# Kernel optimization log

Hardware: AMD Instinct MI355X
Metric: run time of the kernel (lower is better)

Reference implementation:

```python
import jax, jax.numpy as jnp
import numpy as np

jax.config.update("jax_enable_x64", True)  # original torch code runs in float64; minors underflow fp32

D = 96   # Nsites
N = 48   # Nparticles


def setup_inputs() -> dict:
    key = jax.random.key(0)
    # Orthonormal single-particle orbitals (columns), as the module assumes (P^T P = I)
    A = jax.random.normal(key, (D, D), dtype=jnp.float64)
    Q, _ = jnp.linalg.qr(A)
    P = Q[:, :N]  # [D, N]
    # A valid ordered particle configuration: strictly increasing, occ_positions[k] <= D-N+k
    occ_positions = jnp.arange(N, dtype=jnp.int32) * (D // N)  # stride-2 filling
    return {"P": P, "occ_positions": occ_positions}


def _cond_probs(P, occ_positions):
    """Conditional probabilities probs[k, x] of placing the k-th (ordered) particle at
    site x given particles 0..k-1 at occ_positions[0..k-1].

    Math identical to SlaterDetSampler_ordered.get_cond_prob (naive_update=True):
      G = I - P P^T
      probs[k,x] = -det(M_x[0:x+1,0:x+1]) / det(M[0:xmin,0:xmin])
    where M = G - diag(occupancy of particles < k) and M_x additionally sets n_x = 1.
    Since Ksites is always the contiguous range 0..x, all determinants are LEADING
    principal minors; and because only the (x,x) diagonal entry changes by -1 (last index
    of the block), det(M_x block) = d_{x+1} - d_x with d_j the leading j-minor of M.
    """
    Dd, Nn = P.shape
    dt = P.dtype
    eye = jnp.eye(Dd, dtype=dt)
    G = eye - P @ P.T                                             # [D, D]

    onehots = jax.nn.one_hot(occ_positions, Dd, dtype=dt)         # [N, D]
    n_before = jnp.cumsum(onehots, axis=0) - onehots              # occupancy of particles < k
    A = G[None] - n_before[:, :, None] * eye                      # [N, D, D]: G - diag(n_<k)

    # All leading principal minors via batched det of masked matrices:
    # M_j = A on the [0:j,0:j] block, identity elsewhere  =>  det(M_j) = leading j-minor
    ii = jnp.arange(Dd)
    jj = jnp.arange(1, Dd + 1)
    blk = (ii[None, :, None] < jj[:, None, None]) & (ii[None, None, :] < jj[:, None, None])  # [D,D,D]
    Ms = jnp.where(blk[None], A[:, None], eye)                    # [N, D, D, D]
    d = jnp.linalg.det(Ms.reshape(Nn * Dd, Dd, Dd)).reshape(Nn, Dd)
    d_full = jnp.concatenate([jnp.ones((Nn, 1), dt), d], axis=1)  # d_full[k, j] = j-th leading minor

    k = jnp.arange(Nn)
    xmin = jnp.where(k == 0, 0, occ_positions[jnp.maximum(k - 1, 0)] + 1)  # [N]
    xmax = Dd - Nn + k + 1                                                  # [N]
    denom = jnp.take_along_axis(d_full, xmin[:, None], axis=1)              # [N, 1]
    num = d_full[:, 1:] - d_full[:, :-1]                                    # det(GG_num) per candidate x

    x = jnp.arange(Dd)
    support = (x[None, :] >= xmin[:, None]) & (x[None, :] < xmax[:, None])
    probs = jnp.where(support, -num / denom, jnp.zeros((), dt))
    # torch.where(abs(probs) > 1e-15, probs, 0.)
    probs = jnp.where(jnp.abs(probs) > 1e-15, probs, jnp.zeros((), dt))
    return probs


def reference(P, occ_positions):
    probs = _cond_probs(P, occ_positions)                          # [N, D]
    # prob of the full ordered sample = prod_k probs[k, occ_positions[k]]  (as in sample())
    p_k = jnp.take_along_axis(probs, occ_positions[:, None], axis=1)[:, 0]
    prob_sample = jnp.prod(p_k)
    return probs, prob_sample
```

## Files before the change

kernel.cpp:

```cpp
#include <hip/hip_runtime.h>
#include <math.h>

#define Dd 96
#define Nn 48
#define LD 97
#define PTS 98

__device__ __forceinline__ double frcp(double x) {
    double r = __builtin_amdgcn_rcp(x);
    r = fma(fma(-x, r, 1.0), r, r);
    r = fma(fma(-x, r, 1.0), r, r);
    return r;
}

__device__ __forceinline__ double rdlane(double v, int srcLane) {
    union { double d; int i[2]; } u; u.d = v;
    int lo = __builtin_amdgcn_readlane(u.i[0], srcLane);
    int hi = __builtin_amdgcn_readlane(u.i[1], srcLane);
    union { int i[2]; double d; } w; w.i[0] = lo; w.i[1] = hi;
    return w.d;
}

__global__ __launch_bounds__(1024, 1) void slater_kernel(const float* __restrict__ P,
                                                         const int* __restrict__ occ,
                                                         float* __restrict__ out,
                                                         unsigned* __restrict__ cnt) {
    __shared__ double As[Dd * LD];
    __shared__ double Sbuf[2][6][Dd];
    __shared__ double ev[2][6];
    __shared__ int    evmask[2], sdead[2];
    __shared__ double evm[6];
    __shared__ int    evmmask;
    __shared__ double gs_runprod;
    __shared__ int    gs_dead;
    __shared__ unsigned char flag[Dd];
    float* PT = (float*)As;

    const int tid  = threadIdx.x;
    const int k    = blockIdx.x;
    const int n    = Dd - Nn + k + 1;
    const int lane = tid & 63;
    const int wave = tid >> 6;
    const int xmin = (k == 0) ? 0 : occ[k - 1] + 1;

    if (tid < Dd) flag[tid] = 0;
    __syncthreads();
    if (tid < k) flag[occ[tid]] = 1;
    for (int e = tid; e < Dd * Nn; e += 1024) {
        int c = e / Nn, t = e - (e / Nn) * Nn;
        PT[t * PTS + c] = P[e];
    }
    __syncthreads();

    double Areg[8]; int trs[2], tcs[2];
#pragma unroll
    for (int it = 0; it < 2; ++it) {
        int tau = tid + 1024 * it;
        double s00 = 0.0, s01 = 0.0, s10 = 0.0, s11 = 0.0;
        int tr = 0, tc = 0;
        if (tau < 1176) {
            tr = (int)((97.0 - sqrt(9409.0 - 8.0 * (double)tau)) * 0.5);
            while ((tr * (97 - tr)) / 2 > tau) --tr;
            while (((tr + 1) * (96 - tr)) / 2 <= tau) ++tr;
            tc = tr + (tau - (tr * (97 - tr)) / 2);
            int r0 = 2 * tr, c0 = 2 * tc;
            if (r0 < n && c0 < n) {
                for (int t = 0; t < Nn; ++t) {
                    const float* row = PT + t * PTS;
                    float2 pr = *(const float2*)(row + r0);
                    float2 pc = *(const float2*)(row + c0);
                    s00 -= (double)pr.x * (double)pc.x; s01 -= (double)pr.x * (double)pc.y;
                    s10 -= (double)pr.y * (double)pc.x; s11 -= (double)pr.y * (double)pc.y;
                }
            }
        }
        trs[it] = tr; tcs[it] = tc;
        Areg[it * 4 + 0] = s00; Areg[it * 4 + 1] = s01;
        Areg[it * 4 + 2] = s10; Areg[it * 4 + 3] = s11;
    }
    __syncthreads();
#pragma unroll
    for (int it = 0; it < 2; ++it) {
        int tau = tid + 1024 * it;
        if (tau < 1176) {
            int tr = trs[it], tc = tcs[it];
            int r0 = 2 * tr, c0 = 2 * tc;
            if (r0 < n && c0 < n) {
                bool r1 = (r0 + 1 < n), c1 = (c0 + 1 < n);
                double d0 = flag[r0] ? 0.0 : 1.0;
                double d1 = flag[r0 + 1] ? 0.0 : 1.0;
                As[r0 * LD + c0] = Areg[it * 4 + 0] + ((r0 == c0) ? d0 : 0.0);
                if (c1)       As[r0 * LD + c0 + 1]       = Areg[it * 4 + 1];
                if (r1)       As[(r0 + 1) * LD + c0]     = Areg[it * 4 + 2];
                if (r1 && c1) As[(r0 + 1) * LD + c0 + 1] = Areg[it * 4 + 3] + ((r0 == c0) ? d1 : 0.0);
                if (tr != tc) {
                    As[c0 * LD + r0] = Areg[it * 4 + 0];
                    if (c1)       As[(c0 + 1) * LD + r0]     = Areg[it * 4 + 1];
                    if (r1)       As[c0 * LD + r0 + 1]       = Areg[it * 4 + 2];
                    if (r1 && c1) As[(c0 + 1) * LD + r0 + 1] = Areg[it * 4 + 3];
                }
            }
        }
    }
    __syncthreads();

    double myprob = 0.0;
    double rr[6][2];

    auto prefactor = [&](int jb, int p, double grun, int gdead) {
        const int jbH = jb >> 1;
        int msk = 0;
#pragma unroll
        for (int cc = 0; cc < 6; ++cc) {
            const int src = jbH + (cc >> 1);
            double piv = rdlane(rr[cc][cc & 1], src);
            if (!gdead) {
                double ap = fabs(piv);
                int jj = jb + cc;
                if (jj >= xmin) {
                    if (lane == 0) ev[p][cc] = grun * (1.0 - piv);
                    msk |= (1 << cc);
                    double nr = grun * piv;
                    if (!(ap > 1e-7) || !(ap < 8.0) || !(fabs(nr) > 1e-8)) gdead = 1;
                    else grun = nr;
                } else {
                    if (!(ap > 1e-12) || !(ap < 8.0)) gdead = 1;
                }
            }
            double rp = frcp(piv);
            rr[cc][0] *= rp; rr[cc][1] *= rp;
#pragma unroll
            for (int i = 0; i < 6; ++i) {
                if (i == cc) continue;
                double f = rdlane(rr[i][cc & 1], src);
                rr[i][0] -= f * rr[cc][0];
                rr[i][1] -= f * rr[cc][1];
            }
        }
        if (lane == 0) {
            evmask[p] = msk; sdead[p] = gdead;
            gs_runprod = grun; gs_dead = gdead;
        }
        if (lane < 48) {
            const bool live = (2 * lane >= jb + 6);
#pragma unroll
            for (int r = 0; r < 6; ++r) {
                Sbuf[p][r][2 * lane]     = live ? rr[r][0] : 0.0;
                Sbuf[p][r][2 * lane + 1] = live ? rr[r][1] : 0.0;
            }
        }
    };

#pragma unroll
    for (int u = 0; u < 6; ++u) {
        if (lane < 48) {
            rr[u][0] = As[(6 * wave + u) * LD + 2 * lane];
            rr[u][1] = As[(6 * wave + u) * LD + 2 * lane + 1];
        } else { rr[u][0] = 0.0; rr[u][1] = 0.0; }
    }
    if (wave == 0) prefactor(0, 0, 1.0, 0);
    __syncthreads();

    int j = 0, s = 0;
    for (; j + 6 <= n - 1; j += 6, ++s) {
        const int par = s & 1;
        if (tid >= j && tid < j + 6) {
            int q = tid - j;
            if ((evmask[par] >> q) & 1) myprob = ev[par][q];
        }
        if (sdead[par]) break;
        const bool nexts = (j + 12 <= n - 1);

        if (wave >= s + 1 && lane < 48) {
            double S0[6], S1[6];
#pragma unroll
            for (int r = 0; r < 6; ++r) {
                double2 sv = *(const double2*)&Sbuf[par][r][2 * lane];
                S0[r] = sv.x; S1[r] = sv.y;
            }
#pragma unroll
            for (int u = 0; u < 6; ++u) {
#pragma unroll
                for (int r = 0; r < 6; ++r) {
                    double a = rdlane(rr[u][r & 1], 3 * s + (r >> 1));
                    rr[u][0] -= a * S0[r];
                    rr[u][1] -= a * S1[r];
                }
            }
        }
        if (nexts && wave == s + 1)
            prefactor(j + 6, par ^ 1, gs_runprod, gs_dead);
        __syncthreads();
    }

    const int  jend = j;
    const bool full = (jend + 6 > n - 1);
    if (full && wave == (jend / 6)) {
        const int rsz = n - jend;
        const int jeH = jend >> 1;
        double grun = gs_runprod; int gdead = gs_dead;
        int msk = 0;
#pragma unroll
        for (int cc = 0; cc < 6; ++cc) {
            const int src = jeH + (cc >> 1);
            double piv = rdlane(rr[cc][cc & 1], src);
            double evv = 0.0;
            if (cc < rsz - 1) {
                if (!gdead) {
                    double ap = fabs(piv);
                    int jj = jend + cc;
                    if (jj >= xmin) {
                        evv = grun * (1.0 - piv); msk |= (1 << cc);
                        double nr = grun * piv;
                        if (!(ap > 1e-7) || !(ap < 8.0) || !(fabs(nr) > 1e-8)) gdead = 1;
                        else grun = nr;
                    } else {
                        if (!(ap > 1e-12) || !(ap < 8.0)) gdead = 1;
                    }
                }
            } else if (cc == rsz - 1) {
                if (!gdead) { evv = grun * (1.0 - piv); msk |= (1 << cc); }
            }
            if (lane == 0) evm[cc] = evv;
            double rp = frcp(piv);
            rr[cc][0] *= rp; rr[cc][1] *= rp;
#pragma unroll
            for (int i = 0; i < 6; ++i) {
                if (i == cc) continue;
                double f = rdlane(rr[i][cc & 1], src);
                rr[i][0] -= f * rr[cc][0];
                rr[i][1] -= f * rr[cc][1];
            }
        }
        if (lane == 0) evmmask = msk;
    }
    __syncthreads();
    if (full && tid >= jend && tid < n) {
        int q = tid - jend;
        if ((evmmask >> q) & 1) myprob = evm[q];
    }

    if (tid < Dd) {
        double p = myprob;
        if (!isfinite(p)) p = 0.0;
        if (!(fabs(p) > 1e-15)) p = 0.0;
        p = fmin(fmax(p, 0.0), 1.0);
        out[k * Dd + tid] = (float)p;
    }

    __threadfence();
    __syncthreads();
    if (wave == 0) {
        int old = 0;
        if (lane == 0)
            old = (int)__hip_atomic_fetch_add(cnt, 1u, __ATOMIC_ACQ_REL,
                                              __HIP_MEMORY_SCOPE_AGENT);
        old = __shfl(old, 0, 64);
        if (((unsigned)old + 1u) % (unsigned)Nn == 0u) {
            __threadfence();
            double v = 1.0;
            if (lane < Nn) {
                float f = __hip_atomic_load(out + lane * Dd + occ[lane],
                                            __ATOMIC_RELAXED, __HIP_MEMORY_SCOPE_AGENT);
                v = (double)f;
            }
#pragma unroll
            for (int off = 32; off >= 1; off >>= 1)
                v *= __shfl_down(v, off, 64);
            if (lane == 0) {
                if (!isfinite(v)) v = 0.0;
                out[Nn * Dd] = (float)v;
            }
        }
    }
}

extern "C" void kernel_launch(void* const* d_in, const int* in_sizes, int n_in,
                              void* d_out, int out_size, void* d_ws, size_t ws_size,
                              hipStream_t stream) {
    const float* P = (const float*)d_in[0];
    const int* occ = (const int*)d_in[1];
    float* out = (float*)d_out;

    slater_kernel<<<Nn, 1024, 0, stream>>>(P, occ, out, (unsigned*)d_ws);
}
```

Measured before the change: 97.73 us.

## Replace per-step block barriers with flag-based wave pipelining in blocked LU

Drops the __syncthreads between elimination steps in the blocked leading-minor LU. The pivot-panel producer wave now publishes its step through an atomic release counter, and consumer waves spin on it. A 4-slot ring buffer for the panel with per-slot consumption counters lets the producer of later steps run ahead without waiting for every wave. Eigenvalue results are kept per step and gathered once at the end. This is meant to cut barrier stalls on the sequential critical path, at the cost of spin-wait overhead and more complex memory-ordering logic.

```diff
diff --git a/kernel.cpp b/kernel.cpp
--- a/kernel.cpp
+++ b/kernel.cpp
@@ -26,13 +26,15 @@
                                                          float* __restrict__ out,
                                                          unsigned* __restrict__ cnt) {
     __shared__ double As[Dd * LD];
-    __shared__ double Sbuf[2][6][Dd];
-    __shared__ double ev[2][6];
-    __shared__ int    evmask[2], sdead[2];
+    __shared__ double Sbuf[4][6][Dd];
+    __shared__ double ev16[16][6];
+    __shared__ int    evmask16[16], sdead16[16];
     __shared__ double evm[6];
     __shared__ int    evmmask;
     __shared__ double gs_runprod;
     __shared__ int    gs_dead;
+    __shared__ int    step_pub;
+    __shared__ int    done4[4];
     __shared__ unsigned char flag[Dd];
     float* PT = (float*)As;
 
@@ -42,7 +44,12 @@
     const int lane = tid & 63;
     const int wave = tid >> 6;
     const int xmin = (k == 0) ? 0 : occ[k - 1] + 1;
-
+    const int s_end = (n - 1) / 6;
+    const int jend  = 6 * s_end;
+
+    if (tid == 0) { step_pub = -1; gs_runprod = 1.0; gs_dead = 0; evmmask = 0; }
+    if (tid < 4)  done4[tid] = 0;
+    if (tid < 16) { evmask16[tid] = 0; sdead16[tid] = 0; }
     if (tid < Dd) flag[tid] = 0;
     __syncthreads();
     if (tid < k) flag[occ[tid]] = 1;
@@ -107,8 +114,17 @@
     double myprob = 0.0;
     double rr[6][2];
 
-    auto prefactor = [&](int jb, int p, double grun, int gdead) {
-        const int jbH = jb >> 1;
+#pragma unroll
+    for (int u = 0; u < 6; ++u) {
+        if (lane < 48) {
+            rr[u][0] = As[(6 * wave + u) * LD + 2 * lane];
+            rr[u][1] = As[(6 * wave + u) * LD + 2 * lane + 1];
+        } else { rr[u][0] = 0.0; rr[u][1] = 0.0; }
+    }
+
+    auto prefactor = [&](int p, int slot) {
+        const int jb = 6 * p, jbH = 3 * p;
+        double grun = gs_runprod; int gdead = gs_dead;
         int msk = 0;
 #pragma unroll
         for (int cc = 0; cc < 6; ++cc) {
@@ -118,7 +134,7 @@
                 double ap = fabs(piv);
                 int jj = jb + cc;
                 if (jj >= xmin) {
-                    if (lane == 0) ev[p][cc] = grun * (1.0 - piv);
+                    if (lane == 0) ev16[p][cc] = grun * (1.0 - piv);
                     msk |= (1 << cc);
                     double nr = grun * piv;
                     if (!(ap > 1e-7) || !(ap < 8.0) || !(fabs(nr) > 1e-8)) gdead = 1;
@@ -138,71 +154,78 @@
             }
         }
         if (lane == 0) {
-            evmask[p] = msk; sdead[p] = gdead;
+            evmask16[p] = msk; sdead16[p] = gdead;
             gs_runprod = grun; gs_dead = gdead;
         }
         if (lane < 48) {
             const bool live = (2 * lane >= jb + 6);
 #pragma unroll
             for (int r = 0; r < 6; ++r) {
-                Sbuf[p][r][2 * lane]     = live ? rr[r][0] : 0.0;
-                Sbuf[p][r][2 * lane + 1] = live ? rr[r][1] : 0.0;
-            }
-        }
+                double2 sv;
+                sv.x = live ? rr[r][0] : 0.0;
+                sv.y = live ? rr[r][1] : 0.0;
+                *(double2*)&Sbuf[slot][r][2 * lane] = sv;
+            }
+        }
+        __threadfence_block();
+        if (lane == 0)
+            __hip_atomic_store(&step_pub, p, __ATOMIC_RELEASE, __HIP_MEMORY_SCOPE_WORKGROUP);
     };
 
-#pragma unroll
-    for (int u = 0; u < 6; ++u) {
+    if (wave == 0) prefactor(0, 0);
+
+    bool broke = false;
+    const int smax = (wave < s_end) ? wave : s_end;
+    for (int s = 0; s < smax; ++s) {
+        while (__hip_atomic_load(&step_pub, __ATOMIC_ACQUIRE,
+                                 __HIP_MEMORY_SCOPE_WORKGROUP) < s)
+            __builtin_amdgcn_s_sleep(1);
+        if (sdead16[s]) { broke = true; break; }
+        const int slot = s & 3;
+        double S0[6], S1[6];
         if (lane < 48) {
-            rr[u][0] = As[(6 * wave + u) * LD + 2 * lane];
-            rr[u][1] = As[(6 * wave + u) * LD + 2 * lane + 1];
-        } else { rr[u][0] = 0.0; rr[u][1] = 0.0; }
-    }
-    if (wave == 0) prefactor(0, 0, 1.0, 0);
-    __syncthreads();
-
-    int j = 0, s = 0;
-    for (; j + 6 <= n - 1; j += 6, ++s) {
-        const int par = s & 1;
-        if (tid >= j && tid < j + 6) {
-            int q = tid - j;
-            if ((evmask[par] >> q) & 1) myprob = ev[par][q];
-        }
-        if (sdead[par]) break;
-        const bool nexts = (j + 12 <= n - 1);
-
-        if (wave >= s + 1 && lane < 48) {
-            double S0[6], S1[6];
 #pragma unroll
             for (int r = 0; r < 6; ++r) {
-                double2 sv = *(const double2*)&Sbuf[par][r][2 * lane];
+                double2 sv = *(const double2*)&Sbuf[slot][r][2 * lane];
                 S0[r] = sv.x; S1[r] = sv.y;
             }
+        }
+        asm volatile("s_waitcnt lgkmcnt(0)" ::: "memory");
+        if (lane == 0)
+            __hip_atomic_fetch_add(&done4[slot], 1, __ATOMIC_RELAXED,
+                                   __HIP_MEMORY_SCOPE_WORKGROUP);
+        if (lane < 48) {
+            const int al = 3 * s;
 #pragma unroll
             for (int u = 0; u < 6; ++u) {
 #pragma unroll
                 for (int r = 0; r < 6; ++r) {
-                    double a = rdlane(rr[u][r & 1], 3 * s + (r >> 1));
+                    double a = rdlane(rr[u][r & 1], al + (r >> 1));
                     rr[u][0] -= a * S0[r];
                     rr[u][1] -= a * S1[r];
                 }
             }
         }
-        if (nexts && wave == s + 1)
-            prefactor(j + 6, par ^ 1, gs_runprod, gs_dead);
-        __syncthreads();
-    }
-
-    const int  jend = j;
-    const bool full = (jend + 6 > n - 1);
-    if (full && wave == (jend / 6)) {
+        if (wave == s + 1 && s + 1 < s_end) {
+            const int p = s + 1;
+            if (p >= 4) {
+                const int q = p & 3, m = p >> 2;
+                const int T = m * (15 - q) - 2 * m * (m - 1);
+                while (__hip_atomic_load(&done4[q], __ATOMIC_ACQUIRE,
+                                         __HIP_MEMORY_SCOPE_WORKGROUP) < T)
+                    __builtin_amdgcn_s_sleep(1);
+            }
+            prefactor(p, p & 3);
+        }
+    }
+
+    if (!broke && wave == s_end) {
         const int rsz = n - jend;
-        const int jeH = jend >> 1;
         double grun = gs_runprod; int gdead = gs_dead;
         int msk = 0;
 #pragma unroll
         for (int cc = 0; cc < 6; ++cc) {
-            const int src = jeH + (cc >> 1);
+            const int src = 3 * s_end + (cc >> 1);
             double piv = rdlane(rr[cc][cc & 1], src);
             double evv = 0.0;
             if (cc < rsz - 1) {
@@ -235,7 +258,11 @@
         if (lane == 0) evmmask = msk;
     }
     __syncthreads();
-    if (full && tid >= jend && tid < n) {
+
+    if (tid < jend) {
+        int sp = tid / 6, q = tid - 6 * sp;
+        if ((evmask16[sp] >> q) & 1) myprob = ev16[sp][q];
+    } else if (tid < n) {
         int q = tid - jend;
         if ((evmmask >> q) & 1) myprob = evm[q];
     }
```

Result: no change. 96.03 us (-1.7%).
